# Kernel tuning notes

Measured on AMD Instinct MI355X. Metric: run time of the kernel, lower is better.

Reference implementation:

```python
import jax, jax.numpy as jnp
import numpy as np

B, T, I, H, O = 256, 500, 256, 256, 128

def _unif(key, shape, fan):
    bound = 1.0 / np.sqrt(fan)
    return jax.random.uniform(key, shape, jnp.float32, -bound, bound)

def setup_inputs() -> dict:
    key = jax.random.key(0)
    ks = jax.random.split(key, 12)
    return {
        "x": jax.random.normal(ks[0], (B, T, I), jnp.float32),
        # layer 0 (input_dim -> hidden)
        "W_ih0": _unif(ks[1], (H, I), H),
        "W_hh0": _unif(ks[2], (H, H), H),
        "b_ih0": _unif(ks[3], (H,), H),
        "b_hh0": _unif(ks[4], (H,), H),
        # layer 1 (hidden -> hidden)
        "W_ih1": _unif(ks[5], (H, H), H),
        "W_hh1": _unif(ks[6], (H, H), H),
        "b_ih1": _unif(ks[7], (H,), H),
        "b_hh1": _unif(ks[8], (H,), H),
        # fc head
        "fc_W": _unif(ks[9], (O, H), H),
        "fc_b": _unif(ks[10], (O,), H),
    }

def _rnn_layer(x_btf, W_ih, W_hh, b_ih, b_hh):
    # Precompute input projection for all timesteps in one GEMM: [B,T,H]
    xp = jnp.einsum("bti,hi->bth", x_btf, W_ih) + b_ih
    xp = jnp.swapaxes(xp, 0, 1)  # [T,B,H] for scan over time
    h0 = jnp.zeros((xp.shape[1], W_hh.shape[0]), xp.dtype)

    def step(h, xt):
        h_new = jnp.tanh(xt + h @ W_hh.T + b_hh)
        return h_new, h_new

    _, hs = jax.lax.scan(step, h0, xp)  # hs: [T,B,H]
    return jnp.swapaxes(hs, 0, 1)       # [B,T,H]

def reference(x, W_ih0, W_hh0, b_ih0, b_hh0, W_ih1, W_hh1, b_ih1, b_hh1, fc_W, fc_b):
    h1 = _rnn_layer(x, W_ih0, W_hh0, b_ih0, b_hh0)
    h2 = _rnn_layer(h1, W_ih1, W_hh1, b_ih1, b_hh1)
    logits = jnp.einsum("bth,oh->bto", h2, fc_W) + fc_b
    return jax.nn.sigmoid(logits)
```

## Files before the change

kernel.cpp:

```cpp
#include <hip/hip_runtime.h>
#include <hip/hip_fp16.h>

typedef _Float16 half_t;
typedef _Float16 half2_t __attribute__((ext_vector_type(2)));
typedef _Float16 f16x8 __attribute__((ext_vector_type(8)));
typedef float f32x4 __attribute__((ext_vector_type(4)));
typedef unsigned int u32;

#define MROWS 128000
#define KDIM 256
#define TANH_SCALE 2.8853900817779268f

__global__ __launch_bounds__(256) void prep_kernel(
    const float* __restrict__ Wih0, const float* __restrict__ Whh0,
    const float* __restrict__ bih0, const float* __restrict__ bhh0,
    const float* __restrict__ Wih1, const float* __restrict__ Whh1,
    const float* __restrict__ bih1, const float* __restrict__ bhh1,
    const float* __restrict__ fcW,  const float* __restrict__ fcb,
    half_t* __restrict__ Wh0, half_t* __restrict__ Wh1, half_t* __restrict__ fcWh,
    half_t* __restrict__ Whh0h, half_t* __restrict__ Whh1h,
    float* __restrict__ bias0, float* __restrict__ bias1, float* __restrict__ bias2)
{
    const float c = TANH_SCALE;
    int e = blockIdx.x * 256 + threadIdx.x;
    Wh0[e] = (half_t)(Wih0[e] * c);
    Wh1[e] = (half_t)(Wih1[e] * c);
    Whh0h[e] = (half_t)(Whh0[e] * c);
    Whh1h[e] = (half_t)(Whh1[e] * c);
    if (e < 32768) fcWh[e] = (half_t)fcW[e];
    if (e < 256) { bias0[e] = (bih0[e] + bhh0[e]) * c; bias1[e] = (bih1[e] + bhh1[e]) * c; }
    if (e < 128) { bias2[e] = fcb[e]; }
}

template<typename AT, typename OT, int NT, bool SIG>
__global__ __launch_bounds__(512) void gemm_bt(
    const AT* __restrict__ A, const half_t* __restrict__ W,
    const float* __restrict__ bias, OT* __restrict__ C)
{
    constexpr int K = KDIM;
    __shared__ __align__(16) half_t As[128][72];
    __shared__ __align__(16) half_t Ws[NT][72];
    __shared__ float bs[NT];
    const int tid  = threadIdx.x;
    const int row0 = blockIdx.x * 128;
    if (tid < NT) bs[tid] = bias[tid];
    constexpr int NFRAG = NT / 64;
    f32x4 acc[4][NFRAG] = {};
    const int lane = tid & 63;
    const int wid  = tid >> 6;
    const int wr = wid >> 2, wc = wid & 3;

    for (int kt = 0; kt < 4; ++kt) {
        const int k0 = kt * 64;
        if constexpr (sizeof(AT) == 4) {
            #pragma unroll
            for (int p = 0; p < 4; ++p) {
                int idx = p * 512 + tid; int r = idx >> 4; int c4 = (idx & 15) * 4;
                const float4 v = *(const float4*)(A + (size_t)(row0 + r) * K + k0 + c4);
                half2_t h01; h01.x = (half_t)v.x; h01.y = (half_t)v.y;
                half2_t h23; h23.x = (half_t)v.z; h23.y = (half_t)v.w;
                *(half2_t*)&As[r][c4]     = h01;
                *(half2_t*)&As[r][c4 + 2] = h23;
            }
        } else {
            #pragma unroll
            for (int p = 0; p < 2; ++p) {
                int idx = p * 512 + tid; int r = idx >> 3; int c8 = (idx & 7) * 8;
                uint4 v = *(const uint4*)(A + (size_t)(row0 + r) * K + k0 + c8);
                *(uint4*)&As[r][c8] = v;
            }
        }
        #pragma unroll
        for (int p = 0; p < NT / 64; ++p) {
            int idx = p * 512 + tid; int r = idx >> 3; int c8 = (idx & 7) * 8;
            uint4 v = *(const uint4*)(W + (size_t)r * K + k0 + c8);
            *(uint4*)&Ws[r][c8] = v;
        }
        __syncthreads();
        #pragma unroll
        for (int kkh = 0; kkh < 2; ++kkh) {
            const int kk = kkh * 32 + ((lane >> 4) * 8);
            f16x8 af[4], bf[NFRAG];
            #pragma unroll
            for (int m = 0; m < 4; ++m)
                af[m] = *(const f16x8*)&As[wr * 64 + m * 16 + (lane & 15)][kk];
            #pragma unroll
            for (int n = 0; n < NFRAG; ++n)
                bf[n] = *(const f16x8*)&Ws[wc * (NT / 4) + n * 16 + (lane & 15)][kk];
            #pragma unroll
            for (int m = 0; m < 4; ++m)
                #pragma unroll
                for (int n = 0; n < NFRAG; ++n)
                    acc[m][n] = __builtin_amdgcn_mfma_f32_16x16x32_f16(af[m], bf[n], acc[m][n], 0, 0, 0);
        }
        __syncthreads();
    }
    #pragma unroll
    for (int m = 0; m < 4; ++m)
        #pragma unroll
        for (int n = 0; n < NFRAG; ++n)
            #pragma unroll
            for (int jj = 0; jj < 4; ++jj) {
                int rl = wr * 64 + m * 16 + ((lane >> 4) * 4) + jj;
                int cl = wc * (NT / 4) + n * 16 + (lane & 15);
                float v = acc[m][n][jj] + bs[cl];
                if constexpr (SIG) v = 1.0f / (1.0f + __expf(-v));
                C[(size_t)(row0 + rl) * NT + cl] = (OT)v;
            }
}


typedef __attribute__((address_space(1))) const unsigned gu32;
typedef __attribute__((address_space(3))) unsigned lu32;

__device__ __forceinline__ void stage16(const void* g, void* l) {
    __builtin_amdgcn_global_load_lds((gu32*)g, (lu32*)l, 16, 0, 0);
}

__device__ __forceinline__ int swz(int b, int byteoff) {
    return b * 512 + (byteoff ^ ((b & 7) << 4));
}

__device__ __forceinline__ float tanh_pre(float s) {
    float e = __builtin_amdgcn_exp2f(s);
    return __builtin_fmaf(-2.0f, __builtin_amdgcn_rcpf(e + 1.0f), 1.0f);
}

__global__ __launch_bounds__(512, 2) void rnn_fused_scan(
    const half_t* __restrict__ Whh0w,
    const half_t* __restrict__ Wih1w,
    const half_t* __restrict__ Whh1w,
    const float*  __restrict__ bias1,
    const half_t* __restrict__ xp0,
    half_t* __restrict__ h1out)
{
    __shared__ __align__(16) char lds[98304];
    char* const h0t = lds;
    char* const h1t = lds + 16384;
    char* const xs  = lds + 32768;

    const int tid = threadIdx.x;
    const int w = tid >> 6, l = tid & 63, lq = l >> 4, bl = l & 15;
    const bool live = blockIdx.x < 16;
    const int blk = blockIdx.x & 15;

    f16x8 wf0[2][8], wf1[2][8], wh1[2][8];
    #pragma unroll
    for (int m = 0; m < 2; ++m)
        #pragma unroll
        for (int kt = 0; kt < 8; ++kt) {
            const size_t o = (size_t)(w * 32 + m * 16 + bl) * 256 + kt * 32 + lq * 8;
            wf0[m][kt] = *(const f16x8*)(Whh0w + o);
            wf1[m][kt] = *(const f16x8*)(Wih1w + o);
            wh1[m][kt] = *(const f16x8*)(Whh1w + o);
        }
    f32x4 b1f[2];
    #pragma unroll
    for (int m = 0; m < 2; ++m)
        b1f[m] = *(const f32x4*)(bias1 + w * 32 + m * 16 + lq * 4);

    uint4 z = {0u, 0u, 0u, 0u};
    #pragma unroll
    for (int i = 0; i < 4; ++i) ((uint4*)lds)[i * 512 + tid] = z;

    const int r0 = tid >> 5, c0 = (tid & 31) * 16;
    const char* const srcA = (const char*)xp0
        + (size_t)(blk * 16 + r0) * 500 * 512 + (c0 ^ ((r0 & 7) << 4));

    #pragma unroll
    for (int s = 0; s < 4; ++s)
        stage16(srcA + (size_t)s * 512, xs + s * 8192 + w * 1024);

    char* hst = (char*)h1out + ((size_t)(blk * 16 + bl) * 500 * 256 + w * 32 + lq * 4) * 2;

    __syncthreads();

    auto step = [&](int e, char* h0c, char* h0n, char* h1c, char* h1n,
                    bool doL0, bool doL1) {
        {
            const int tc = (e + 4 > 499) ? 499 : (e + 4);
            stage16(srcA + (size_t)tc * 512, xs + (size_t)((e + 4) & 7) * 8192 + w * 1024);
        }
        f32x4 acc0[2] = {};
        f32x4 acc1[2] = {b1f[0], b1f[1]};
        {
            f16x8 bf0[8];
            #pragma unroll
            for (int kt = 0; kt < 8; ++kt)
                bf0[kt] = *(const f16x8*)(h0c + swz(bl, kt * 64 + lq * 16));
            #pragma unroll
            for (int kt = 0; kt < 8; ++kt)
                #pragma unroll
                for (int m = 0; m < 2; ++m) {
                    acc0[m] = __builtin_amdgcn_mfma_f32_16x16x32_f16(wf0[m][kt], bf0[kt], acc0[m], 0, 0, 0);
                    acc1[m] = __builtin_amdgcn_mfma_f32_16x16x32_f16(wf1[m][kt], bf0[kt], acc1[m], 0, 0, 0);
                }
        }
        {
            f16x8 bf1[8];
            #pragma unroll
            for (int kt = 0; kt < 8; ++kt)
                bf1[kt] = *(const f16x8*)(h1c + swz(bl, kt * 64 + lq * 16));
            #pragma unroll
            for (int kt = 0; kt < 8; ++kt)
                #pragma unroll
                for (int m = 0; m < 2; ++m)
                    acc1[m] = __builtin_amdgcn_mfma_f32_16x16x32_f16(wh1[m][kt], bf1[kt], acc1[m], 0, 0, 0);
        }
        if (doL0) {
            const char* xcur = xs + (size_t)(e & 7) * 8192;
            #pragma unroll
            for (int m = 0; m < 2; ++m) {
                const int off = w * 64 + m * 32 + lq * 8;
                uint2 xv = *(const uint2*)(xcur + swz(bl, off));
                const half_t* xh = (const half_t*)&xv;
                float v0 = tanh_pre(acc0[m][0] + (float)xh[0]);
                float v1 = tanh_pre(acc0[m][1] + (float)xh[1]);
                float v2 = tanh_pre(acc0[m][2] + (float)xh[2]);
                float v3 = tanh_pre(acc0[m][3] + (float)xh[3]);
                uint2 hv;
                hv.x = __builtin_bit_cast(u32, __builtin_amdgcn_cvt_pkrtz(v0, v1));
                hv.y = __builtin_bit_cast(u32, __builtin_amdgcn_cvt_pkrtz(v2, v3));
                *(uint2*)(h0n + swz(bl, off)) = hv;
            }
        }
        if (doL1) {
            #pragma unroll
            for (int m = 0; m < 2; ++m) {
                const int off = w * 64 + m * 32 + lq * 8;
                float v0 = tanh_pre(acc1[m][0]);
                float v1 = tanh_pre(acc1[m][1]);
                float v2 = tanh_pre(acc1[m][2]);
                float v3 = tanh_pre(acc1[m][3]);
                uint2 hv;
                hv.x = __builtin_bit_cast(u32, __builtin_amdgcn_cvt_pkrtz(v0, v1));
                hv.y = __builtin_bit_cast(u32, __builtin_amdgcn_cvt_pkrtz(v2, v3));
                *(uint2*)(h1n + swz(bl, off)) = hv;
                if (live) *(uint2*)(hst + m * 32) = hv;
            }
            hst += 512;
        }
        if (live) asm volatile("s_waitcnt vmcnt(8) lgkmcnt(0)\n\ts_barrier" ::: "memory");
        else      asm volatile("s_waitcnt vmcnt(3) lgkmcnt(0)\n\ts_barrier" ::: "memory");
    };

    step(0, h0t, h0t + 8192, h1t, h1t + 8192, true, false);
    for (int i = 0; i < 249; ++i) {
        const int e = 2 * i + 1;
        step(e,     h0t + 8192, h0t, h1t + 8192, h1t, true, true);
        step(e + 1, h0t, h0t + 8192, h1t, h1t + 8192, true, true);
    }
    step(499, h0t + 8192, h0t, h1t + 8192, h1t, true, true);
    step(500, h0t, h0t + 8192, h1t, h1t + 8192, false, true);
}

extern "C" void kernel_launch(void* const* d_in, const int* in_sizes, int n_in,
                              void* d_out, int out_size, void* d_ws, size_t ws_size,
                              hipStream_t stream) {
    const float* x    = (const float*)d_in[0];
    const float* Wih0 = (const float*)d_in[1];
    const float* Whh0 = (const float*)d_in[2];
    const float* bih0 = (const float*)d_in[3];
    const float* bhh0 = (const float*)d_in[4];
    const float* Wih1 = (const float*)d_in[5];
    const float* Whh1 = (const float*)d_in[6];
    const float* bih1 = (const float*)d_in[7];
    const float* bhh1 = (const float*)d_in[8];
    const float* fcW  = (const float*)d_in[9];
    const float* fcb  = (const float*)d_in[10];

    char* ws = (char*)d_ws;
    size_t off = 0;
    auto alloc = [&](size_t bytes) { void* p = ws + off; off += (bytes + 255) & ~(size_t)255; return p; };
    half_t* xp_buf = (half_t*)alloc((size_t)MROWS * 256 * 2);
    half_t* h_buf  = (half_t*)alloc((size_t)MROWS * 256 * 2);
    half_t* Wh0    = (half_t*)alloc(65536 * 2);
    half_t* Wh1    = (half_t*)alloc(65536 * 2);
    half_t* fcWh   = (half_t*)alloc(32768 * 2);
    half_t* Whh0h  = (half_t*)alloc(65536 * 2);
    half_t* Whh1h  = (half_t*)alloc(65536 * 2);
    float*  bias0  = (float*)alloc(256 * 4);
    float*  bias1  = (float*)alloc(256 * 4);
    float*  bias2  = (float*)alloc(128 * 4);

    prep_kernel<<<256, 256, 0, stream>>>(Wih0, Whh0, bih0, bhh0, Wih1, Whh1, bih1, bhh1,
                                         fcW, fcb, Wh0, Wh1, fcWh, Whh0h, Whh1h,
                                         bias0, bias1, bias2);
    gemm_bt<float, half_t, 256, false><<<1000, 512, 0, stream>>>(x, Wh0, bias0, xp_buf);
    rnn_fused_scan<<<256, 512, 0, stream>>>(Whh0h, Wh1, Whh1h, bias1, xp_buf, h_buf);
    gemm_bt<half_t, float, 128, true><<<1000, 512, 0, stream>>>(h_buf, fcWh, bias2, (float*)d_out);
}
```

Baseline: 764.9 us.

## Pin weight fragments in registers, split LDS B-loads, raise MFMA priority

Empty asm constraints pin the weight fragments and bias so the compiler keeps them in VGPRs instead of rematerializing or spilling them. The per-step B-operand LDS loads are split into two halves of four to cut live registers. The MFMA section runs at raised wave priority. The vmcnt wait threshold for live blocks is relaxed so more global stores can stay in flight at the barrier. These target register pressure and latency on the serial recurrence, at the risk of wrong vmcnt accounting or extra LDS load latency exposed between halves.

```diff
diff --git a/kernel.cpp b/kernel.cpp
--- a/kernel.cpp
+++ b/kernel.cpp
@@ -6,6 +6,7 @@
 typedef _Float16 f16x8 __attribute__((ext_vector_type(8)));
 typedef float f32x4 __attribute__((ext_vector_type(4)));
 typedef unsigned int u32;
+typedef u32 u32x4v __attribute__((ext_vector_type(4)));
 
 #define MROWS 128000
 #define KDIM 256
@@ -121,6 +122,12 @@
     return b * 512 + (byteoff ^ ((b & 7) << 4));
 }
 
+__device__ __forceinline__ void pin8(f16x8& v) {
+    u32x4v t = __builtin_bit_cast(u32x4v, v);
+    asm volatile("" : "+v"(t));
+    v = __builtin_bit_cast(f16x8, t);
+}
+
 __device__ __forceinline__ float tanh_pre(float s) {
     float e = __builtin_amdgcn_exp2f(s);
     return __builtin_fmaf(-2.0f, __builtin_amdgcn_rcpf(e + 1.0f), 1.0f);
@@ -154,10 +161,18 @@
             wf1[m][kt] = *(const f16x8*)(Wih1w + o);
             wh1[m][kt] = *(const f16x8*)(Whh1w + o);
         }
+    #pragma unroll
+    for (int m = 0; m < 2; ++m)
+        #pragma unroll
+        for (int kt = 0; kt < 8; ++kt) {
+            pin8(wf0[m][kt]); pin8(wf1[m][kt]); pin8(wh1[m][kt]);
+        }
     f32x4 b1f[2];
     #pragma unroll
-    for (int m = 0; m < 2; ++m)
+    for (int m = 0; m < 2; ++m) {
         b1f[m] = *(const f32x4*)(bias1 + w * 32 + m * 16 + lq * 4);
+        asm volatile("" : "+v"(b1f[m]));
+    }
 
     uint4 z = {0u, 0u, 0u, 0u};
     #pragma unroll
@@ -183,30 +198,50 @@
         }
         f32x4 acc0[2] = {};
         f32x4 acc1[2] = {b1f[0], b1f[1]};
+        __builtin_amdgcn_s_setprio(1);
         {
-            f16x8 bf0[8];
-            #pragma unroll
-            for (int kt = 0; kt < 8; ++kt)
-                bf0[kt] = *(const f16x8*)(h0c + swz(bl, kt * 64 + lq * 16));
-            #pragma unroll
-            for (int kt = 0; kt < 8; ++kt)
+            f16x8 bf[4];
+            #pragma unroll
+            for (int kt = 0; kt < 4; ++kt)
+                bf[kt] = *(const f16x8*)(h0c + swz(bl, kt * 64 + lq * 16));
+            #pragma unroll
+            for (int kt = 0; kt < 4; ++kt)
                 #pragma unroll
                 for (int m = 0; m < 2; ++m) {
-                    acc0[m] = __builtin_amdgcn_mfma_f32_16x16x32_f16(wf0[m][kt], bf0[kt], acc0[m], 0, 0, 0);
-                    acc1[m] = __builtin_amdgcn_mfma_f32_16x16x32_f16(wf1[m][kt], bf0[kt], acc1[m], 0, 0, 0);
+                    acc0[m] = __builtin_amdgcn_mfma_f32_16x16x32_f16(wf0[m][kt], bf[kt], acc0[m], 0, 0, 0);
+                    acc1[m] = __builtin_amdgcn_mfma_f32_16x16x32_f16(wf1[m][kt], bf[kt], acc1[m], 0, 0, 0);
                 }
+            #pragma unroll
+            for (int kt = 0; kt < 4; ++kt)
+                bf[kt] = *(const f16x8*)(h0c + swz(bl, (kt + 4) * 64 + lq * 16));
+            #pragma unroll
+            for (int kt = 0; kt < 4; ++kt)
+                #pragma unroll
+                for (int m = 0; m < 2; ++m) {
+                    acc0[m] = __builtin_amdgcn_mfma_f32_16x16x32_f16(wf0[m][kt + 4], bf[kt], acc0[m], 0, 0, 0);
+                    acc1[m] = __builtin_amdgcn_mfma_f32_16x16x32_f16(wf1[m][kt + 4], bf[kt], acc1[m], 0, 0, 0);
+                }
         }
         {
-            f16x8 bf1[8];
-            #pragma unroll
-            for (int kt = 0; kt < 8; ++kt)
-                bf1[kt] = *(const f16x8*)(h1c + swz(bl, kt * 64 + lq * 16));
-            #pragma unroll
-            for (int kt = 0; kt < 8; ++kt)
+            f16x8 bf[4];
+            #pragma unroll
+            for (int kt = 0; kt < 4; ++kt)
+                bf[kt] = *(const f16x8*)(h1c + swz(bl, kt * 64 + lq * 16));
+            #pragma unroll
+            for (int kt = 0; kt < 4; ++kt)
                 #pragma unroll
                 for (int m = 0; m < 2; ++m)
-                    acc1[m] = __builtin_amdgcn_mfma_f32_16x16x32_f16(wh1[m][kt], bf1[kt], acc1[m], 0, 0, 0);
-        }
+                    acc1[m] = __builtin_amdgcn_mfma_f32_16x16x32_f16(wh1[m][kt], bf[kt], acc1[m], 0, 0, 0);
+            #pragma unroll
+            for (int kt = 0; kt < 4; ++kt)
+                bf[kt] = *(const f16x8*)(h1c + swz(bl, (kt + 4) * 64 + lq * 16));
+            #pragma unroll
+            for (int kt = 0; kt < 4; ++kt)
+                #pragma unroll
+                for (int m = 0; m < 2; ++m)
+                    acc1[m] = __builtin_amdgcn_mfma_f32_16x16x32_f16(wh1[m][kt + 4], bf[kt], acc1[m], 0, 0, 0);
+        }
+        __builtin_amdgcn_s_setprio(0);
         if (doL0) {
             const char* xcur = xs + (size_t)(e & 7) * 8192;
             #pragma unroll
@@ -240,7 +275,7 @@
             }
             hst += 512;
         }
-        if (live) asm volatile("s_waitcnt vmcnt(8) lgkmcnt(0)\n\ts_barrier" ::: "memory");
+        if (live) asm volatile("s_waitcnt vmcnt(11) lgkmcnt(0)\n\ts_barrier" ::: "memory");
         else      asm volatile("s_waitcnt vmcnt(3) lgkmcnt(0)\n\ts_barrier" ::: "memory");
     };
 
```

Result: slower. 801.8 us (+4.8%).
